# Kernel optimization log

Measured on AMD Instinct MI355X. Metric: run time of the kernel, lower is better.

Reference implementation:

```python
import jax, jax.numpy as jnp
import numpy as np

LN_EPS = 1e-5


def setup_inputs() -> dict:
    key = jax.random.key(0)
    ks = jax.random.split(key, 6)
    B, L, N, H, V = 4, 4, 2048, 64, 4
    x = jax.random.normal(ks[0], (B, N, H), dtype=jnp.float32)
    feature = jax.random.normal(ks[1], (B, N, 2), dtype=jnp.float32)
    adj = jax.random.uniform(ks[2], (B, L, N, N), dtype=jnp.float32)
    fc_w = jax.random.normal(ks[3], (H, H + 2), dtype=jnp.float32) * (1.0 / np.sqrt(H + 2))
    fc_b = jnp.zeros((H,), dtype=jnp.float32)
    ln_g = jnp.ones((H,), dtype=jnp.float32)
    ln_b = jnp.zeros((H,), dtype=jnp.float32)
    W = jax.random.normal(ks[4], (H, V, H), dtype=jnp.float32) * (1.0 / np.sqrt(H))
    a = jax.random.normal(ks[5], (L + 1, V), dtype=jnp.float32) * 0.5
    return {"x": x, "feature": feature, "adj": adj, "fc_w": fc_w, "fc_b": fc_b,
            "ln_g": ln_g, "ln_b": ln_b, "W": W, "a": a}


def reference(x, feature, adj, fc_w, fc_b, ln_g, ln_b, W, a):
    # x: [B,N,H], feature: [B,N,2], adj: [B,L,N,N]
    label_plus1 = a.shape[0]  # label_num + 1
    h = jnp.concatenate([x, feature], axis=2) @ fc_w.T + fc_b  # [B,N,H]
    mu = jnp.mean(h, axis=-1, keepdims=True)
    var = jnp.var(h, axis=-1, keepdims=True)
    h = (h - mu) / jnp.sqrt(var + LN_EPS) * ln_g + ln_b
    h = jnp.tanh(h)  # dropout inactive in eval mode
    # supports: identity relation (h itself) + one bmm per adjacency label
    prop = jnp.einsum('blnm,bmd->blnd', adj, h)            # [B,L,N,H]
    supports = jnp.concatenate([h[:, None], prop], axis=1)  # [B,L+1,N,H]
    # combine learned per-label weights: a @ W -> [L+1, H, H]
    M = jnp.einsum('lv,dve->lde', a, W)
    out = jnp.einsum('blnd,lde->bne', supports, M) / label_plus1  # sum over labels
    return out + x  # residual with original x
```

## Files before the change

### kernel.cpp

```cpp
#include <hip/hip_runtime.h>
#include <stdint.h>

#define BB 4
#define LL 4
#define NN 2048
#define HH 64

typedef __attribute__((ext_vector_type(4))) float  f32x4;
typedef __attribute__((ext_vector_type(8))) short  short8;

static __device__ __forceinline__ uint16_t f2bf(float f) {
    uint32_t u = __float_as_uint(f);
    u += 0x7FFFu + ((u >> 16) & 1u);
    return (uint16_t)(u >> 16);
}

__global__ __launch_bounds__(256) void prep_kernel(
    const float* __restrict__ x, const float* __restrict__ feat,
    const float* __restrict__ fc_w, const float* __restrict__ fc_b,
    const float* __restrict__ ln_g, const float* __restrict__ ln_b,
    const float* __restrict__ W, const float* __restrict__ a,
    float* __restrict__ out, uint16_t* __restrict__ zT)
{
    __shared__ float    sW[64 * 67];
    __shared__ uint16_t sM[5 * 64 * 64];

    const int tid = threadIdx.x;

    for (int i = tid; i < 64 * 66; i += 256) {
        int d = i / 66, k = i - d * 66;
        sW[d * 67 + k] = fc_w[i];
    }
    for (int i = tid; i < 5 * 64 * 64; i += 256) {
        int l = i >> 12;
        int d = (i >> 6) & 63;
        int e = i & 63;
        const float* wp = W + (size_t)(d * 4) * 64 + e;
        float acc = a[l * 4 + 0] * wp[0]   + a[l * 4 + 1] * wp[64]
                  + a[l * 4 + 2] * wp[128] + a[l * 4 + 3] * wp[192];
        sM[i] = f2bf(acc);
    }
    __syncthreads();

    const int wave = tid >> 6, lane = tid & 63;
    const int row0 = blockIdx.x * 32 + wave * 8;
    const int b    = row0 >> 11;
    const int m0   = row0 & 2047;

    const float fcb = fc_b[lane], lng = ln_g[lane], lnb = ln_b[lane];

    float xv[8], hv[8];
#pragma unroll
    for (int r = 0; r < 8; r++) {
        const int row = row0 + r;
        xv[r] = x[(size_t)row * 64 + lane];
        const float f0 = feat[row * 2 + 0];
        const float f1 = feat[row * 2 + 1];
        float acc = fcb;
#pragma unroll
        for (int k = 0; k < 64; k++)
            acc += __shfl(xv[r], k) * sW[lane * 67 + k];
        acc += f0 * sW[lane * 67 + 64] + f1 * sW[lane * 67 + 65];
        float s = acc, s2 = acc * acc;
#pragma unroll
        for (int off = 32; off > 0; off >>= 1) {
            s  += __shfl_xor(s,  off);
            s2 += __shfl_xor(s2, off);
        }
        const float mean = s * (1.0f / 64.0f);
        const float var  = s2 * (1.0f / 64.0f) - mean * mean;
        const float y = (acc - mean) * rsqrtf(var + 1e-5f) * lng + lnb;
        hv[r] = tanhf(y);
    }

    float accz[5][8];
#pragma unroll
    for (int l = 0; l < 5; l++)
#pragma unroll
        for (int r = 0; r < 8; r++) accz[l][r] = 0.0f;

    for (int d = 0; d < 64; d++) {
        float hb[8];
#pragma unroll
        for (int r = 0; r < 8; r++) hb[r] = __shfl(hv[r], d);
#pragma unroll
        for (int l = 0; l < 5; l++) {
            const float mv =
                __uint_as_float(((uint32_t)sM[(l << 12) + (d << 6) + lane]) << 16);
#pragma unroll
            for (int r = 0; r < 8; r++) accz[l][r] += hb[r] * mv;
        }
    }

#pragma unroll
    for (int r = 0; r < 8; r++)
        out[(size_t)(row0 + r) * 64 + lane] = xv[r] + 0.2f * accz[0][r];

#pragma unroll
    for (int l = 1; l < 5; l++) {
        uint32_t w0 = (uint32_t)f2bf(accz[l][0]) | ((uint32_t)f2bf(accz[l][1]) << 16);
        uint32_t w1 = (uint32_t)f2bf(accz[l][2]) | ((uint32_t)f2bf(accz[l][3]) << 16);
        uint32_t w2 = (uint32_t)f2bf(accz[l][4]) | ((uint32_t)f2bf(accz[l][5]) << 16);
        uint32_t w3 = (uint32_t)f2bf(accz[l][6]) | ((uint32_t)f2bf(accz[l][7]) << 16);
        uint4* dst = (uint4*)(zT + (((size_t)(b * 4 + (l - 1)) * 64 + lane) * 2048 + m0));
        *dst = make_uint4(w0, w1, w2, w3);
    }
}

__global__ __launch_bounds__(64) void gemm_kernel(
    const float* __restrict__ adj, const uint16_t* __restrict__ zT,
    float* __restrict__ out)
{
    const int blk = blockIdx.x;
    const int ks  = blk & 1;
    const int rt  = (blk >> 1) & 63;
    const int l   = (blk >> 7) & 3;
    const int b   = blk >> 9;

    const int lane = threadIdx.x;
    const int q    = lane >> 4;
    const int mr   = lane & 15;

    const int n0 = rt * 32;
    const int k0 = ks * 1024;

    const float* adjBase = adj + ((size_t)(b * 4 + l) * 2048) * 2048;
    const float* aRow0 = adjBase + (size_t)(n0 + mr) * 2048 + k0 + q * 8;
    const float* aRow1 = aRow0 + (size_t)16 * 2048;
    const uint16_t* zCol =
        zT + ((size_t)(b * 4 + l) * 64 + mr) * 2048 + k0 + q * 8;

    f32x4 acc[2][4];
#pragma unroll
    for (int i = 0; i < 2; i++)
#pragma unroll
        for (int j = 0; j < 4; j++) acc[i][j] = (f32x4){0.f, 0.f, 0.f, 0.f};

    f32x4  af[2][2][2];
    short8 bq[2][4];

#define LOADSTEP(pp, s) do {                                                  \
        const float* _a0 = aRow0 + (s) * 32;                                  \
        const float* _a1 = aRow1 + (s) * 32;                                  \
        af[pp][0][0] = *(const f32x4*)(_a0);                                  \
        af[pp][0][1] = *(const f32x4*)(_a0 + 4);                              \
        af[pp][1][0] = *(const f32x4*)(_a1);                                  \
        af[pp][1][1] = *(const f32x4*)(_a1 + 4);                              \
        const uint16_t* _z = zCol + (s) * 32;                                 \
        bq[pp][0] = *(const short8*)(_z);                                     \
        bq[pp][1] = *(const short8*)(_z + 16 * 2048);                         \
        bq[pp][2] = *(const short8*)(_z + 32 * 2048);                         \
        bq[pp][3] = *(const short8*)(_z + 48 * 2048);                         \
    } while (0)

#define COMPUTE(pp) do {                                                      \
        short8 _fa0, _fa1;                                                    \
        _Pragma("unroll")                                                     \
        for (int j = 0; j < 4; j++) {                                         \
            _fa0[j]     = (short)f2bf(af[pp][0][0][j]);                       \
            _fa0[j + 4] = (short)f2bf(af[pp][0][1][j]);                       \
            _fa1[j]     = (short)f2bf(af[pp][1][0][j]);                       \
            _fa1[j + 4] = (short)f2bf(af[pp][1][1][j]);                       \
        }                                                                     \
        _Pragma("unroll")                                                     \
        for (int et = 0; et < 4; et++) {                                      \
            acc[0][et] = __builtin_amdgcn_mfma_f32_16x16x32_bf16(             \
                _fa0, bq[pp][et], acc[0][et], 0, 0, 0);                       \
            acc[1][et] = __builtin_amdgcn_mfma_f32_16x16x32_bf16(             \
                _fa1, bq[pp][et], acc[1][et], 0, 0, 0);                       \
        }                                                                     \
    } while (0)

    LOADSTEP(0, 0);
    for (int s = 0; s < 30; s += 2) {
        LOADSTEP(1, s + 1);
        COMPUTE(0);
        LOADSTEP(0, s + 2);
        COMPUTE(1);
    }
    LOADSTEP(1, 31);
    COMPUTE(0);
    COMPUTE(1);

#undef LOADSTEP
#undef COMPUTE

#pragma unroll
    for (int f = 0; f < 2; f++)
#pragma unroll
        for (int et = 0; et < 4; et++)
#pragma unroll
            for (int r = 0; r < 4; r++) {
                const int row = n0 + f * 16 + q * 4 + r;
                const int col = et * 16 + mr;
                atomicAdd(out + ((size_t)b * 2048 + row) * 64 + col,
                          0.2f * acc[f][et][r]);
            }
}

extern "C" void kernel_launch(void* const* d_in, const int* in_sizes, int n_in,
                              void* d_out, int out_size, void* d_ws, size_t ws_size,
                              hipStream_t stream) {
    const float* x    = (const float*)d_in[0];
    const float* feat = (const float*)d_in[1];
    const float* adj  = (const float*)d_in[2];
    const float* fc_w = (const float*)d_in[3];
    const float* fc_b = (const float*)d_in[4];
    const float* ln_g = (const float*)d_in[5];
    const float* ln_b = (const float*)d_in[6];
    const float* W    = (const float*)d_in[7];
    const float* a    = (const float*)d_in[8];

    float*    out = (float*)d_out;
    uint16_t* zT  = (uint16_t*)d_ws;

    prep_kernel<<<256, 256, 0, stream>>>(x, feat, fc_w, fc_b, ln_g, ln_b,
                                         W, a, out, zT);
    gemm_kernel<<<2048, 64, 0, stream>>>(adj, zT, out);
}
```

Baseline: 445.4 us.

## Reduce label partials in shared memory instead of global atomics

The GEMM kernel now uses 256-thread blocks where each wave handles one adjacency label over the full K range, replacing split-K across blocks. The four label partials are summed through shared memory and added to the output with vectorized read-modify-write, removing all global atomics. This cuts the grid from 2048 single-wave blocks to 256 four-wave blocks, which lowers parallelism and lengthens each wave's serial loop over a memory-bound fp32 adjacency stream.

```diff
diff --git a/kernel.cpp b/kernel.cpp
--- a/kernel.cpp
+++ b/kernel.cpp
@@ -107,28 +107,28 @@
     }
 }
 
-__global__ __launch_bounds__(64) void gemm_kernel(
+__global__ __launch_bounds__(256) void gemm_kernel(
     const float* __restrict__ adj, const uint16_t* __restrict__ zT,
     float* __restrict__ out)
 {
+    __shared__ float sAcc[4][32 * 64];
+
     const int blk = blockIdx.x;
-    const int ks  = blk & 1;
-    const int rt  = (blk >> 1) & 63;
-    const int l   = (blk >> 7) & 3;
-    const int b   = blk >> 9;
-
-    const int lane = threadIdx.x;
+    const int rt  = blk & 63;
+    const int b   = blk >> 6;
+
+    const int wave = threadIdx.x >> 6;
+    const int lane = threadIdx.x & 63;
     const int q    = lane >> 4;
     const int mr   = lane & 15;
 
     const int n0 = rt * 32;
-    const int k0 = ks * 1024;
-
-    const float* adjBase = adj + ((size_t)(b * 4 + l) * 2048) * 2048;
-    const float* aRow0 = adjBase + (size_t)(n0 + mr) * 2048 + k0 + q * 8;
+
+    const float* adjBase = adj + ((size_t)(b * 4 + wave) * 2048) * 2048;
+    const float* aRow0 = adjBase + (size_t)(n0 + mr) * 2048 + q * 8;
     const float* aRow1 = aRow0 + (size_t)16 * 2048;
     const uint16_t* zCol =
-        zT + ((size_t)(b * 4 + l) * 64 + mr) * 2048 + k0 + q * 8;
+        zT + ((size_t)(b * 4 + wave) * 64 + mr) * 2048 + q * 8;
 
     f32x4 acc[2][4];
 #pragma unroll
@@ -172,13 +172,13 @@
     } while (0)
 
     LOADSTEP(0, 0);
-    for (int s = 0; s < 30; s += 2) {
+    for (int s = 0; s < 62; s += 2) {
         LOADSTEP(1, s + 1);
         COMPUTE(0);
         LOADSTEP(0, s + 2);
         COMPUTE(1);
     }
-    LOADSTEP(1, 31);
+    LOADSTEP(1, 63);
     COMPUTE(0);
     COMPUTE(1);
 
@@ -190,12 +190,26 @@
 #pragma unroll
         for (int et = 0; et < 4; et++)
 #pragma unroll
-            for (int r = 0; r < 4; r++) {
-                const int row = n0 + f * 16 + q * 4 + r;
-                const int col = et * 16 + mr;
-                atomicAdd(out + ((size_t)b * 2048 + row) * 64 + col,
-                          0.2f * acc[f][et][r]);
-            }
+            for (int r = 0; r < 4; r++)
+                sAcc[wave][(f * 16 + q * 4 + r) * 64 + et * 16 + mr] =
+                    acc[f][et][r];
+    __syncthreads();
+
+    const int t    = threadIdx.x;
+    const int row  = t >> 3;
+    const int col0 = (t & 7) * 8;
+    const int lo   = row * 64 + col0;
+    float* op = out + ((size_t)b * 2048 + n0 + row) * 64 + col0;
+#pragma unroll
+    for (int p = 0; p < 2; p++) {
+        f32x4 s = *(const f32x4*)&sAcc[0][lo + p * 4];
+        s = s + *(const f32x4*)&sAcc[1][lo + p * 4];
+        s = s + *(const f32x4*)&sAcc[2][lo + p * 4];
+        s = s + *(const f32x4*)&sAcc[3][lo + p * 4];
+        f32x4 o = *(f32x4*)(op + p * 4);
+        o = o + 0.2f * s;
+        *(f32x4*)(op + p * 4) = o;
+    }
 }
 
 extern "C" void kernel_launch(void* const* d_in, const int* in_sizes, int n_in,
@@ -216,5 +230,5 @@
 
     prep_kernel<<<256, 256, 0, stream>>>(x, feat, fc_w, fc_b, ln_g, ln_b,
                                          W, a, out, zT);
-    gemm_kernel<<<2048, 64, 0, stream>>>(adj, zT, out);
-}
+    gemm_kernel<<<256, 256, 0, stream>>>(adj, zT, out);
+}
```

Result: no change. 444.2 us (-0.3%).
